# Optimization experiments

Measured on AMD Instinct MI355X. Metric: run time of the kernel, lower is better.

The kernel has to match this reference:

```python
import jax, jax.numpy as jnp
import numpy as np

N_NODES = 100000
N_EDGES = 400000
N_GRAPHS = 2048
F_IN = 78
HEADS1 = 10
OUT2 = 128


def _gat_conv(x, src, dst, W, a_src, a_dst, b, heads, out_dim):
    """PyG-style GATConv with self-loops already included in (src, dst)."""
    N = x.shape[0]
    h = (x @ W).reshape(N, heads, out_dim)                       # [N,H,D]
    alpha_src = jnp.einsum('nhd,hd->nh', h, a_src)               # [N,H]
    alpha_dst = jnp.einsum('nhd,hd->nh', h, a_dst)               # [N,H]
    e = jax.nn.leaky_relu(alpha_src[src] + alpha_dst[dst], 0.2)  # [E,H]
    # ragged softmax over incoming edges per destination node
    m = jax.ops.segment_max(e, dst, num_segments=N)
    m = jnp.where(jnp.isfinite(m), m, 0.0)
    ex = jnp.exp(e - jax.lax.stop_gradient(m)[dst])
    denom = jax.ops.segment_sum(ex, dst, num_segments=N)
    alpha = ex / (denom[dst] + 1e-16)                            # [E,H]
    msg = h[src] * alpha[:, :, None]                             # [E,H,D]
    out = jax.ops.segment_sum(msg, dst, num_segments=N)          # [N,H,D]
    return out.reshape(N, heads * out_dim) + b


def setup_inputs() -> dict:
    key = jax.random.key(0)
    ks = jax.random.split(key, 24)
    p = lambda k, shape: (jax.random.normal(k, shape, dtype=jnp.float32) * 0.05)
    x = jax.random.normal(ks[0], (N_NODES, F_IN), dtype=jnp.float32)
    edge_index = jax.random.randint(ks[1], (2, N_EDGES), 0, N_NODES, dtype=jnp.int32)
    # sorted batch assignment guaranteeing every graph is non-empty
    batch = ((jnp.arange(N_NODES, dtype=jnp.int32) * N_GRAPHS) // N_NODES).astype(jnp.int32)
    target = jax.random.normal(ks[2], (N_GRAPHS, 1280), dtype=jnp.float32)
    return {
        'x': x, 'edge_index': edge_index, 'batch': batch, 'target': target,
        'W1': p(ks[3], (F_IN, HEADS1 * F_IN)),
        'a_src1': p(ks[4], (HEADS1, F_IN)),
        'a_dst1': p(ks[5], (HEADS1, F_IN)),
        'b1': jnp.zeros((HEADS1 * F_IN,), jnp.float32),
        'W2': p(ks[6], (HEADS1 * F_IN, OUT2)),
        'a_src2': p(ks[7], (1, OUT2)),
        'a_dst2': p(ks[8], (1, OUT2)),
        'b2': jnp.zeros((OUT2,), jnp.float32),
        'w_gate': p(ks[9], (OUT2, 1)),
        'b_gate': jnp.zeros((1,), jnp.float32),
        'W_xt': p(ks[10], (1280, 256)),
        'b_xt': jnp.zeros((256,), jnp.float32),
        'W_fc1': p(ks[11], (512, 1024)),
        'b_fc1': jnp.zeros((1024,), jnp.float32),
        'W_fc2': p(ks[12], (1024, 256)),
        'b_fc2': jnp.zeros((256,), jnp.float32),
        'W_out': p(ks[13], (256, 1)),
        'b_out': jnp.zeros((1,), jnp.float32),
    }


def reference(x, edge_index, batch, target, W1, a_src1, a_dst1, b1,
              W2, a_src2, a_dst2, b2, w_gate, b_gate, W_xt, b_xt,
              W_fc1, b_fc1, W_fc2, b_fc2, W_out, b_out):
    N = x.shape[0]
    loop = jnp.arange(N, dtype=edge_index.dtype)
    src = jnp.concatenate([edge_index[0], loop])   # add self-loops (PyG default)
    dst = jnp.concatenate([edge_index[1], loop])

    h = jax.nn.elu(_gat_conv(x, src, dst, W1, a_src1, a_dst1, b1, HEADS1, F_IN))
    h = _gat_conv(h, src, dst, W2, a_src2, a_dst2, b2, 1, OUT2)
    h = jax.nn.relu(h)                              # [N,128]

    # WeightedSumAndMax readout
    w = jax.nn.sigmoid(h @ w_gate + b_gate)         # [N,1]
    h_sum = jax.ops.segment_sum(h * w, batch, num_segments=N_GRAPHS)  # [B,128]
    h_max = jax.ops.segment_max(h, batch, num_segments=N_GRAPHS)     # [B,128]
    hg = jnp.concatenate([h_sum, h_max], axis=1)    # [B,256]

    xt = target @ W_xt + b_xt                       # [B,256]
    xc = jnp.concatenate([hg, xt], axis=1)          # [B,512]
    xc = jax.nn.relu(xc @ W_fc1 + b_fc1)
    xc = jax.nn.relu(xc @ W_fc2 + b_fc2)
    return xc @ W_out + b_out                       # [B,1]
```

## Files before the change

kernel.cpp:

```cpp
#include <hip/hip_runtime.h>
#include <cstdint>
#include <cstddef>

#define N_NODESC 100000
#define N_EDGESC 400000
#define N_GRAPHSC 2048
#define F_INC 78
#define HEADS1C 10
#define D1C 78
#define F1C 780
#define OUT2C 128
#define E_TOTC (N_EDGESC + N_NODESC)

typedef unsigned short ushort_t;
typedef __attribute__((ext_vector_type(8))) short short8;
typedef __attribute__((ext_vector_type(4))) float f32x4;
typedef __attribute__((ext_vector_type(4))) unsigned int uint4v;
union U4S8 { uint4v u; short8 s; };

static __device__ __forceinline__ float lrelu(float x){ return x > 0.f ? x : 0.2f*x; }

static __device__ __forceinline__ float elu_fast(float v){
  return (v > 0.f) ? v : (__expf(v) - 1.0f);
}

static __device__ __forceinline__ unsigned short f2bf(float f){
  unsigned int u = __float_as_uint(f);
  unsigned int r = (u + 0x7fffu + ((u >> 16) & 1u)) >> 16;
  return (unsigned short)r;
}
static __device__ __forceinline__ float bf2f(unsigned short h){
  return __uint_as_float(((unsigned int)h) << 16);
}

__global__ void k_deg(const int* __restrict__ ei, int* __restrict__ deg){
  int e = blockIdx.x*256 + threadIdx.x;
  if (e >= E_TOTC) return;
  int dst = (e < N_EDGESC) ? ei[N_EDGESC + e] : (e - N_EDGESC);
  atomicAdd(&deg[dst], 1);
}

__global__ __launch_bounds__(1024) void k_scan1(const int* __restrict__ deg,
                                                int* __restrict__ rowptr,
                                                int* __restrict__ bsum){
  __shared__ int s[1024];
  int t = threadIdx.x, i = blockIdx.x*1024 + t;
  int v = (i < N_NODESC) ? deg[i] : 0;
  s[t] = v; __syncthreads();
  for (int d = 1; d < 1024; d <<= 1){
    int xv = (t >= d) ? s[t-d] : 0;
    __syncthreads();
    s[t] += xv;
    __syncthreads();
  }
  if (i < N_NODESC) rowptr[i+1] = s[t];
  if (t == 1023) bsum[blockIdx.x] = s[t];
}

__global__ void k_scan2(int* __restrict__ bsum, int* __restrict__ rowptr, int nb){
  if (threadIdx.x == 0 && blockIdx.x == 0){
    int run = 0;
    for (int b = 0; b < nb; b++){ int v = bsum[b]; bsum[b] = run; run += v; }
    rowptr[0] = 0;
  }
}

__global__ __launch_bounds__(1024) void k_scan3(int* __restrict__ rowptr,
                                                const int* __restrict__ bsum){
  int i = blockIdx.x*1024 + threadIdx.x;
  if (i < N_NODESC) rowptr[i+1] += bsum[blockIdx.x];
}

__global__ void k_scatter(const int* __restrict__ ei, const int* __restrict__ rowptr,
                          int* __restrict__ cnt, int* __restrict__ esrc){
  int e = blockIdx.x*256 + threadIdx.x;
  if (e >= E_TOTC) return;
  int src, dst;
  if (e < N_EDGESC){ src = ei[e]; dst = ei[N_EDGESC + e]; }
  else { src = dst = e - N_EDGESC; }
  int pos = rowptr[dst] + atomicAdd(&cnt[dst], 1);
  esrc[pos] = src;
}

__global__ void k_wa1(const float* __restrict__ W1, const float* __restrict__ a_src1,
                      const float* __restrict__ a_dst1, float* __restrict__ Wa1){
  int i = blockIdx.x*256 + threadIdx.x;
  if (i >= F_INC*2*HEADS1C) return;
  int d = i / (2*HEADS1C), c = i % (2*HEADS1C);
  const float* a = (c < HEADS1C) ? a_src1 : a_dst1;
  int h = (c < HEADS1C) ? c : c - HEADS1C;
  float s = 0.f;
  for (int j = 0; j < D1C; j++) s += W1[d*F1C + h*D1C + j] * a[h*D1C + j];
  Wa1[d*(2*HEADS1C) + c] = s;
}

__global__ void k_att1(const float* __restrict__ x, const float* __restrict__ Wa1,
                       float* __restrict__ att1){
  int i = blockIdx.x*256 + threadIdx.x;
  if (i >= N_NODESC*2*HEADS1C) return;
  int n = i / (2*HEADS1C), c = i % (2*HEADS1C);
  const float* xr = x + (size_t)n*F_INC;
  float s = 0.f;
  for (int d = 0; d < F_INC; d++) s += xr[d] * Wa1[d*(2*HEADS1C) + c];
  att1[i] = s;
}

__global__ void k_stats1(const float* __restrict__ att1, const int* __restrict__ rowptr,
                         const int* __restrict__ esrc, float* __restrict__ stat1){
  int i = blockIdx.x*256 + threadIdx.x;
  if (i >= N_NODESC*HEADS1C) return;
  int n = i / HEADS1C, h = i % HEADS1C;
  float ad = att1[n*20 + 10 + h];
  int b = rowptr[n], e = rowptr[n+1];
  float m = -1e30f;
  for (int p = b; p < e; p += 4){
    int c = e - p; if (c > 4) c = 4;
    float v[4];
    #pragma unroll
    for (int j = 0; j < 4; j++){ int s = esrc[p + (j < c ? j : 0)]; v[j] = att1[s*20 + h]; }
    #pragma unroll
    for (int j = 0; j < 4; j++) if (j < c) m = fmaxf(m, lrelu(v[j] + ad));
  }
  float den = 0.f;
  for (int p = b; p < e; p += 4){
    int c = e - p; if (c > 4) c = 4;
    float v[4];
    #pragma unroll
    for (int j = 0; j < 4; j++){ int s = esrc[p + (j < c ? j : 0)]; v[j] = att1[s*20 + h]; }
    #pragma unroll
    for (int j = 0; j < 4; j++) if (j < c) den += expf(lrelu(v[j] + ad) - m);
  }
  stat1[n*20 + h] = m;
  stat1[n*20 + 10 + h] = 1.f/(den + 1e-16f);
}

__global__ __launch_bounds__(64) void k_agg1(
    const float* __restrict__ x, const float* __restrict__ att1,
    const float* __restrict__ stat1, const int* __restrict__ rowptr,
    const int* __restrict__ esrc, ushort_t* __restrict__ zc, int base){
  __shared__ float xs[4][F_INC];
  __shared__ float al[4][HEADS1C];
  int n = base + blockIdx.x;
  int l = threadIdx.x;
  int b = rowptr[n], e = rowptr[n+1];
  float acc[13];
  #pragma unroll
  for (int k = 0; k < 13; k++) acc[k] = 0.f;
  int hk[13], dk[13];
  #pragma unroll
  for (int k = 0; k < 13; k++){ int f = l + 64*k; hk[k] = f/78; dk[k] = f%78; }
  float ad = 0.f, mm = 0.f, rd = 0.f;
  if (l < HEADS1C){
    ad = att1[n*20 + 10 + l];
    mm = stat1[n*20 + l];
    rd = stat1[n*20 + 10 + l];
  }
  for (int p = b; p < e; p += 4){
    int c = e - p; if (c > 4) c = 4;
    int ss[4];
    #pragma unroll
    for (int j = 0; j < 4; j++) ss[j] = esrc[p + (j < c ? j : 0)];
    if (l < 39){
      #pragma unroll
      for (int j = 0; j < 4; j++){
        float2 v = *(const float2*)(x + (size_t)ss[j]*F_INC + 2*l);
        xs[j][2*l] = v.x; xs[j][2*l+1] = v.y;
      }
    }
    if (l < HEADS1C){
      #pragma unroll
      for (int j = 0; j < 4; j++){
        float ev = lrelu(att1[ss[j]*20 + l] + ad);
        al[j][l] = (j < c) ? expf(ev - mm) * rd : 0.f;
      }
    }
    __syncthreads();
    #pragma unroll
    for (int k = 0; k < 13; k++){
      int f = l + 64*k;
      if (f < F1C){
        float s = al[0][hk[k]]*xs[0][dk[k]] + al[1][hk[k]]*xs[1][dk[k]]
                + al[2][hk[k]]*xs[2][dk[k]] + al[3][hk[k]]*xs[3][dk[k]];
        acc[k] += s;
      }
    }
    __syncthreads();
  }
  #pragma unroll
  for (int k = 0; k < 13; k++){
    int f = l + 64*k;
    if (f < F1C) zc[(size_t)blockIdx.x*F1C + f] = f2bf(acc[k]);
  }
}

__global__ void k_prepW1(const float* __restrict__ W1, ushort_t* __restrict__ W1t){
  int i = blockIdx.x*256 + threadIdx.x;
  if (i >= HEADS1C*80*96) return;
  int h = i / (80*96), rem = i % (80*96), n = rem / 96, k = rem % 96;
  float v = (n < D1C && k < F_INC) ? W1[(size_t)k*F1C + h*D1C + n] : 0.f;
  W1t[i] = f2bf(v);
}

__global__ void k_prepW2f(const float* __restrict__ W2, ushort_t* __restrict__ W2f){
  int i = blockIdx.x*256 + threadIdx.x;
  if (i >= HEADS1C*128*96) return;
  int h = i / (128*96), rem = i % (128*96), n = rem / 96, k = rem % 96;
  float v = (k < D1C) ? W2[(size_t)(h*D1C + k)*OUT2C + n] : 0.f;
  W2f[i] = f2bf(v);
}

__global__ void k_prepWt(const float* __restrict__ W, ushort_t* __restrict__ Wt,
                         int Kdim, int Ndim, int KB){
  int i = blockIdx.x*256 + threadIdx.x;
  if (i >= Ndim*KB) return;
  int n = i / KB, k = i % KB;
  float v = (k < Kdim) ? W[(size_t)k*Ndim + n] : 0.f;
  Wt[i] = f2bf(v);
}

__global__ void k_cast_bf(const float* __restrict__ in, ushort_t* __restrict__ o, int n){
  int i = blockIdx.x*256 + threadIdx.x;
  if (i < n) o[i] = f2bf(in[i]);
}

template<int BN, int NT, int KB, int KVAL, int ACT, bool HASBIAS>
__global__ __launch_bounds__(256) void mfma_gemm(
    const ushort_t* __restrict__ A, const ushort_t* __restrict__ Bt,
    const float* __restrict__ bias, ushort_t* __restrict__ C,
    int M, int N, int lda, int ldc,
    int zsA, int zsBt, int zsC, int zsBias)
{
  __shared__ unsigned int As[64][20];
  __shared__ unsigned int Bs[BN][20];
  int z = blockIdx.z;
  A += (size_t)z*zsA; Bt += (size_t)z*zsBt; C += (size_t)z*zsC;
  const float* bz = HASBIAS ? (bias + (size_t)z*zsBias) : nullptr;
  int m0 = blockIdx.x*64;
  int n0 = blockIdx.y*BN;
  int t = threadIdx.x;
  int w = t >> 6, lane = t & 63;
  int q = lane >> 4, li = lane & 15;
  f32x4 acc[NT];
  #pragma unroll
  for (int i = 0; i < NT; i++) acc[i] = (f32x4){0.f,0.f,0.f,0.f};

  int am = t >> 2;
  int ak0 = (t & 3)*8;
  int gm = m0 + am;
  bool rv = (gm < M);

  #pragma unroll
  for (int ki = 0; ki < KB/32; ki++){
    const int kt = ki*32;
    int nv;
    if (ki == KB/32 - 1){
      int d = KVAL - ak0; nv = d < 0 ? 0 : (d > 8 ? 8 : d);
    } else nv = 8;
    {
      unsigned u0=0u, u1=0u, u2=0u, u3=0u;
      if (rv && nv > 0){
        const unsigned int* ap = (const unsigned int*)(A + (size_t)gm*lda + kt + ak0);
        u0 = ap[0]; u1 = ap[1]; u2 = ap[2]; u3 = ap[3];
        int ndw = nv >> 1;
        if (ndw < 4) u3 = 0u;
        if (ndw < 3) u2 = 0u;
        if (ndw < 2) u1 = 0u;
      }
      int c0 = (t & 3)*4;
      As[am][c0] = u0; As[am][c0+1] = u1; As[am][c0+2] = u2; As[am][c0+3] = u3;
    }
    for (int g = t; g < BN*4; g += 256){
      int n = g >> 2, c0 = (g & 3)*4;
      const unsigned int* bp = (const unsigned int*)(Bt + (size_t)(n0 + n)*KB + kt + c0*2);
      Bs[n][c0] = bp[0]; Bs[n][c0+1] = bp[1]; Bs[n][c0+2] = bp[2]; Bs[n][c0+3] = bp[3];
    }
    __syncthreads();
    U4S8 a; a.u = *(const uint4v*)&As[w*16 + li][q*4];
    #pragma unroll
    for (int nt = 0; nt < NT; nt++){
      U4S8 b; b.u = *(const uint4v*)&Bs[nt*16 + li][q*4];
      acc[nt] = __builtin_amdgcn_mfma_f32_16x16x32_bf16(a.s, b.s, acc[nt], 0, 0, 0);
    }
    __syncthreads();
  }
  #pragma unroll
  for (int nt = 0; nt < NT; nt++){
    int col = n0 + nt*16 + li;
    if (col >= N) continue;
    float bv = HASBIAS ? bz[col] : 0.f;
    #pragma unroll
    for (int r = 0; r < 4; r++){
      int gmr = m0 + w*16 + q*4 + r;
      if (gmr >= M) continue;
      float v = acc[nt][r] + bv;
      if (ACT == 1) v = fmaxf(v, 0.f);
      else if (ACT == 2) v = (v > 0.f) ? v : (__expf(v) - 1.0f);
      C[(size_t)gmr*ldc + col] = f2bf(v);
    }
  }
}

__global__ __launch_bounds__(256, 4) void mfma_fused12(
    const ushort_t* __restrict__ zc, const ushort_t* __restrict__ W1t,
    const float* __restrict__ b1, const ushort_t* __restrict__ W2f,
    ushort_t* __restrict__ h2pre, float* __restrict__ att2,
    const float* __restrict__ a_src2, const float* __restrict__ a_dst2,
    int M)
{
  __shared__ unsigned int Bs[128][52];
  __shared__ unsigned int Ts[64][52];
  int m0 = blockIdx.x*64;
  int t = threadIdx.x;
  int w = t >> 6, lane = t & 63;
  int q = lane >> 4, li = lane & 15;

  f32x4 acc2[8];
  #pragma unroll
  for (int i = 0; i < 8; i++) acc2[i] = (f32x4){0.f,0.f,0.f,0.f};

  for (int i = t; i < 64*9; i += 256) Ts[i/9][39 + i%9] = 0u;

  int ar = m0 + w*16 + li;
  bool rv = (ar < M);
  const unsigned int* abase = (const unsigned int*)(zc + (size_t)ar*F1C);

  auto lda = [&](int h, uint4v* af){
    af[0] = (uint4v){0u,0u,0u,0u};
    af[1] = (uint4v){0u,0u,0u,0u};
    af[2] = (uint4v){0u,0u,0u,0u};
    if (rv){
      const unsigned int* p = abase + h*39 + q*4;
      af[0][0]=p[0];  af[0][1]=p[1];  af[0][2]=p[2];  af[0][3]=p[3];
      af[1][0]=p[16]; af[1][1]=p[17]; af[1][2]=p[18]; af[1][3]=p[19];
      if (q < 2){
        af[2][0]=p[32]; af[2][1]=p[33]; af[2][2]=p[34]; af[2][3]=p[35];
        if (q == 1) af[2][3] = 0u;
      }
    }
  };

  uint4v acur[3], anxt[3];
  lda(0, acur);

  #pragma unroll 1
  for (int h = 0; h < HEADS1C; h++){
    lda(h+1 < HEADS1C ? h+1 : 0, anxt);

    __syncthreads();
    {
      const unsigned int* bp = (const unsigned int*)(W1t + (size_t)h*80*96);
      #pragma unroll
      for (int g0 = 0; g0 < 4; g0++){
        int g = t + g0*256;
        if (g < 960){
          int n = g/12, c0 = (g%12)*4;
          const unsigned int* p = bp + g*4;
          Bs[n][c0] = p[0]; Bs[n][c0+1] = p[1]; Bs[n][c0+2] = p[2]; Bs[n][c0+3] = p[3];
        }
      }
    }
    float bv[5];
    #pragma unroll
    for (int nt = 0; nt < 5; nt++){
      int col = nt*16 + li;
      bv[nt] = (col < D1C) ? b1[h*D1C + col] : 0.f;
    }
    __syncthreads();

    f32x4 acc1[5];
    #pragma unroll
    for (int i = 0; i < 5; i++) acc1[i] = (f32x4){0.f,0.f,0.f,0.f};
    #pragma unroll
    for (int ki = 0; ki < 3; ki++){
      U4S8 a; a.u = acur[ki];
      #pragma unroll
      for (int nt = 0; nt < 5; nt++){
        U4S8 b; b.u = *(const uint4v*)&Bs[nt*16 + li][ki*16 + q*4];
        acc1[nt] = __builtin_amdgcn_mfma_f32_16x16x32_bf16(a.s, b.s, acc1[nt], 0, 0, 0);
      }
    }
    #pragma unroll
    for (int nt = 0; nt < 5; nt++){
      int col = nt*16 + li;
      #pragma unroll
      for (int r = 0; r < 4; r++){
        int row = w*16 + q*4 + r;
        float v = elu_fast(acc1[nt][r] + bv[nt]);
        ((ushort_t*)&Ts[row][0])[col] = f2bf(v);
      }
    }
    __syncthreads();

    {
      const unsigned int* bp = (const unsigned int*)(W2f + (size_t)h*128*96);
      #pragma unroll
      for (int g0 = 0; g0 < 6; g0++){
        int g = t + g0*256;
        int n = g/12, c0 = (g%12)*4;
        const unsigned int* p = bp + g*4;
        Bs[n][c0] = p[0]; Bs[n][c0+1] = p[1]; Bs[n][c0+2] = p[2]; Bs[n][c0+3] = p[3];
      }
    }
    __syncthreads();

    #pragma unroll
    for (int ki = 0; ki < 3; ki++){
      U4S8 a; a.u = *(const uint4v*)&Ts[w*16 + li][ki*16 + q*4];
      #pragma unroll
      for (int nt = 0; nt < 8; nt++){
        U4S8 b; b.u = *(const uint4v*)&Bs[nt*16 + li][ki*16 + q*4];
        acc2[nt] = __builtin_amdgcn_mfma_f32_16x16x32_bf16(a.s, b.s, acc2[nt], 0, 0, 0);
      }
    }
    acur[0] = anxt[0]; acur[1] = anxt[1]; acur[2] = anxt[2];
  }

  float as2[8], ad2[8];
  #pragma unroll
  for (int nt = 0; nt < 8; nt++){
    int col = nt*16 + li;
    as2[nt] = a_src2[col];
    ad2[nt] = a_dst2[col];
  }
  #pragma unroll
  for (int r = 0; r < 4; r++){
    int gmr = m0 + w*16 + q*4 + r;
    float p0 = 0.f, p1 = 0.f;
    ushort_t hv[8];
    #pragma unroll
    for (int nt = 0; nt < 8; nt++){
      ushort_t hb = f2bf(acc2[nt][r]);
      float vb = bf2f(hb);
      p0 += vb*as2[nt]; p1 += vb*ad2[nt];
      hv[nt] = hb;
    }
    #pragma unroll
    for (int off = 1; off < 16; off <<= 1){
      p0 += __shfl_xor(p0, off);
      p1 += __shfl_xor(p1, off);
    }
    if (gmr < M){
      #pragma unroll
      for (int nt = 0; nt < 8; nt++)
        h2pre[(size_t)gmr*OUT2C + nt*16 + li] = hv[nt];
      if (li == 0){
        att2[(size_t)gmr*2]     = p0;
        att2[(size_t)gmr*2 + 1] = p1;
      }
    }
  }
}

__global__ void k_stats2(const float* __restrict__ att2, const int* __restrict__ rowptr,
                         const int* __restrict__ esrc, float* __restrict__ stat2){
  int n = blockIdx.x*256 + threadIdx.x;
  if (n >= N_NODESC) return;
  float ad = att2[n*2+1];
  int b = rowptr[n], e = rowptr[n+1];
  float m = -1e30f;
  for (int p = b; p < e; p += 4){
    int c = e - p; if (c > 4) c = 4;
    float v[4];
    #pragma unroll
    for (int j = 0; j < 4; j++){ int s = esrc[p + (j < c ? j : 0)]; v[j] = att2[s*2]; }
    #pragma unroll
    for (int j = 0; j < 4; j++) if (j < c) m = fmaxf(m, lrelu(v[j] + ad));
  }
  float den = 0.f;
  for (int p = b; p < e; p += 4){
    int c = e - p; if (c > 4) c = 4;
    float v[4];
    #pragma unroll
    for (int j = 0; j < 4; j++){ int s = esrc[p + (j < c ? j : 0)]; v[j] = att2[s*2]; }
    #pragma unroll
    for (int j = 0; j < 4; j++) if (j < c) den += expf(lrelu(v[j] + ad) - m);
  }
  stat2[n*2] = m;
  stat2[n*2+1] = 1.f/(den + 1e-16f);
}

__global__ void k_agg2(const ushort_t* __restrict__ h2pre,
                       const float* __restrict__ att2,
                       const float* __restrict__ stat2, const int* __restrict__ rowptr,
                       const int* __restrict__ esrc, const float* __restrict__ b2,
                       const float* __restrict__ w_gate, const float* __restrict__ b_gate,
                       float* __restrict__ h2, float* __restrict__ wnode){
  int n = blockIdx.x*4 + (threadIdx.x >> 6);
  int l = threadIdx.x & 63;
  if (n >= N_NODESC) return;
  float ad = att2[n*2+1], m = stat2[n*2], rd = stat2[n*2+1];
  int b = rowptr[n], e = rowptr[n+1];
  float a0 = 0.f, a1 = 0.f;
  for (int p = b; p < e; p += 4){
    int c = e - p; if (c > 4) c = 4;
    int ss[4];
    #pragma unroll
    for (int j = 0; j < 4; j++) ss[j] = esrc[p + (j < c ? j : 0)];
    unsigned u[4]; float at[4];
    #pragma unroll
    for (int j = 0; j < 4; j++) u[j] = *(const unsigned*)(h2pre + (size_t)ss[j]*OUT2C + 2*l);
    #pragma unroll
    for (int j = 0; j < 4; j++) at[j] = att2[ss[j]*2];
    #pragma unroll
    for (int j = 0; j < 4; j++){
      if (j < c){
        float alpha = expf(lrelu(at[j] + ad) - m) * rd;
        a0 += alpha * bf2f((ushort_t)(u[j] & 0xffffu));
        a1 += alpha * bf2f((ushort_t)(u[j] >> 16));
      }
    }
  }
  float v0 = fmaxf(a0 + b2[2*l],   0.f);
  float v1 = fmaxf(a1 + b2[2*l+1], 0.f);
  float2 hv; hv.x = v0; hv.y = v1;
  *(float2*)(h2 + (size_t)n*OUT2C + 2*l) = hv;
  float pp = v0*w_gate[2*l] + v1*w_gate[2*l+1];
  #pragma unroll
  for (int off = 32; off; off >>= 1) pp += __shfl_xor(pp, off);
  if (l == 0) wnode[n] = 1.f/(1.f + expf(-(pp + b_gate[0])));
}

__global__ __launch_bounds__(128) void k_readout(const float* __restrict__ h2,
                                                 const float* __restrict__ wnode,
                                                 const int* __restrict__ batch,
                                                 ushort_t* __restrict__ xcb){
  __shared__ int lohi[2];
  int g = blockIdx.x, t = threadIdx.x;
  if (t == 0){
    int lo = 0, hi = N_NODESC;
    while (lo < hi){ int mid = (lo+hi) >> 1; if (batch[mid] < g) lo = mid+1; else hi = mid; }
    lohi[0] = lo;
    int lo2 = lo; hi = N_NODESC;
    while (lo2 < hi){ int mid = (lo2+hi) >> 1; if (batch[mid] < g+1) lo2 = mid+1; else hi = mid; }
    lohi[1] = lo2;
  }
  __syncthreads();
  int lo = lohi[0], hi = lohi[1];
  float sum = 0.f, mx = 0.f;
  for (int n = lo; n < hi; n++){
    float v = h2[(size_t)n*OUT2C + t];
    sum += v * wnode[n];
    mx = fmaxf(mx, v);
  }
  xcb[(size_t)g*512 + t] = f2bf(sum);
  xcb[(size_t)g*512 + 128 + t] = f2bf(mx);
}

__global__ void k_final(const ushort_t* __restrict__ f2b, const float* __restrict__ W_out,
                        const float* __restrict__ b_out, float* __restrict__ out){
  int g = blockIdx.x*4 + (threadIdx.x >> 6);
  int l = threadIdx.x & 63;
  if (g >= N_GRAPHSC) return;
  float s = 0.f;
  #pragma unroll
  for (int k = 0; k < 4; k++) s += bf2f(f2b[(size_t)g*256 + l + 64*k]) * W_out[l + 64*k];
  #pragma unroll
  for (int off = 32; off; off >>= 1) s += __shfl_xor(s, off);
  if (l == 0) out[g] = s + b_out[0];
}

extern "C" void kernel_launch(void* const* d_in, const int* in_sizes, int n_in,
                              void* d_out, int out_size, void* d_ws, size_t ws_size,
                              hipStream_t stream) {
  const float* x      = (const float*)d_in[0];
  const int*   ei     = (const int*)d_in[1];
  const int*   batch  = (const int*)d_in[2];
  const float* target = (const float*)d_in[3];
  const float* W1     = (const float*)d_in[4];
  const float* a_src1 = (const float*)d_in[5];
  const float* a_dst1 = (const float*)d_in[6];
  const float* b1     = (const float*)d_in[7];
  const float* W2     = (const float*)d_in[8];
  const float* a_src2 = (const float*)d_in[9];
  const float* a_dst2 = (const float*)d_in[10];
  const float* b2     = (const float*)d_in[11];
  const float* w_gate = (const float*)d_in[12];
  const float* b_gate = (const float*)d_in[13];
  const float* W_xt   = (const float*)d_in[14];
  const float* b_xt   = (const float*)d_in[15];
  const float* W_fc1  = (const float*)d_in[16];
  const float* b_fc1  = (const float*)d_in[17];
  const float* W_fc2  = (const float*)d_in[18];
  const float* b_fc2  = (const float*)d_in[19];
  const float* W_out  = (const float*)d_in[20];
  const float* b_out  = (const float*)d_in[21];
  float* out = (float*)d_out;

  const size_t MB = (size_t)1 << 20;
  int C;
  if      (ws_size >= 245*MB) C = 1;
  else if (ws_size >= 150*MB) C = 2;
  else                        C = 4;
  const int R = N_NODESC / C;

  char* p = (char*)d_ws;
  auto carve = [&](size_t bytes) -> char* {
    char* r = p; p += (bytes + 255) & ~(size_t)255; return r;
  };
  int*   deg    = (int*)  carve((size_t)N_NODESC*4);
  int*   rowptr = (int*)  carve((size_t)(N_NODESC+1)*4);
  int*   cnt    = (int*)  carve((size_t)N_NODESC*4);
  int*   esrc   = (int*)  carve((size_t)E_TOTC*4);
  int*   bsum   = (int*)  carve(128*4);
  float* Wa1    = (float*)carve((size_t)F_INC*20*4);
  float* att1   = (float*)carve((size_t)N_NODESC*20*4);
  float* stat1  = (float*)carve((size_t)N_NODESC*20*4);
  float* att2   = (float*)carve((size_t)N_NODESC*2*4);
  float* stat2  = (float*)carve((size_t)N_NODESC*2*4);
  float* wnode  = (float*)carve((size_t)N_NODESC*4);
  ushort_t* W1t   = (ushort_t*)carve((size_t)HEADS1C*80*96*2);
  ushort_t* W2f   = (ushort_t*)carve((size_t)HEADS1C*128*96*2);
  ushort_t* Wxtt  = (ushort_t*)carve((size_t)256*1280*2);
  ushort_t* Wfc1t = (ushort_t*)carve((size_t)1024*512*2);
  ushort_t* Wfc2t = (ushort_t*)carve((size_t)256*1024*2);
  ushort_t* tb    = (ushort_t*)carve((size_t)N_GRAPHSC*1280*2);
  ushort_t* h2pre = (ushort_t*)carve((size_t)N_NODESC*OUT2C*2);
  ushort_t* xcb   = (ushort_t*)carve((size_t)N_GRAPHSC*512*2);
  ushort_t* f1b   = (ushort_t*)carve((size_t)N_GRAPHSC*1024*2);
  ushort_t* f2b   = (ushort_t*)carve((size_t)N_GRAPHSC*256*2);
  size_t big_bytes = (size_t)R*F1C*2 + 4096;
  size_t h2_bytes  = (size_t)N_NODESC*OUT2C*4;
  char*  BIG = carve(big_bytes > h2_bytes ? big_bytes : h2_bytes);
  ushort_t* zc  = (ushort_t*)BIG;
  float* h2 = (float*)BIG;

  hipMemsetAsync(deg, 0, (size_t)N_NODESC*4, stream);
  hipMemsetAsync(cnt, 0, (size_t)N_NODESC*4, stream);

  k_deg<<<(E_TOTC+255)/256, 256, 0, stream>>>(ei, deg);
  int nb = (N_NODESC + 1023)/1024;
  k_scan1<<<nb, 1024, 0, stream>>>(deg, rowptr, bsum);
  k_scan2<<<1, 64, 0, stream>>>(bsum, rowptr, nb);
  k_scan3<<<nb, 1024, 0, stream>>>(rowptr, bsum);
  k_scatter<<<(E_TOTC+255)/256, 256, 0, stream>>>(ei, rowptr, cnt, esrc);

  k_prepW1<<<(HEADS1C*80*96+255)/256, 256, 0, stream>>>(W1, W1t);
  k_prepW2f<<<(HEADS1C*128*96+255)/256, 256, 0, stream>>>(W2, W2f);
  k_prepWt<<<(256*1280+255)/256, 256, 0, stream>>>(W_xt, Wxtt, 1280, 256, 1280);
  k_prepWt<<<(1024*512+255)/256, 256, 0, stream>>>(W_fc1, Wfc1t, 512, 1024, 512);
  k_prepWt<<<(256*1024+255)/256, 256, 0, stream>>>(W_fc2, Wfc2t, 1024, 256, 1024);
  k_cast_bf<<<((N_GRAPHSC*1280)+255)/256, 256, 0, stream>>>(target, tb, N_GRAPHSC*1280);

  k_wa1<<<(F_INC*20+255)/256, 256, 0, stream>>>(W1, a_src1, a_dst1, Wa1);
  k_att1<<<(N_NODESC*20+255)/256, 256, 0, stream>>>(x, Wa1, att1);
  k_stats1<<<(N_NODESC*HEADS1C+255)/256, 256, 0, stream>>>(att1, rowptr, esrc, stat1);

  for (int c = 0; c < C; c++){
    int base = c*R;
    k_agg1<<<R, 64, 0, stream>>>(x, att1, stat1, rowptr, esrc, zc, base);
    mfma_fused12<<<(R+63)/64, 256, 0, stream>>>(
        zc, W1t, b1, W2f, h2pre + (size_t)base*OUT2C, att2 + (size_t)base*2,
        a_src2, a_dst2, R);
  }

  k_stats2<<<(N_NODESC+255)/256, 256, 0, stream>>>(att2, rowptr, esrc, stat2);
  k_agg2<<<(N_NODESC+3)/4, 256, 0, stream>>>(h2pre, att2, stat2, rowptr, esrc,
                                             b2, w_gate, b_gate, h2, wnode);

  k_readout<<<N_GRAPHSC, 128, 0, stream>>>(h2, wnode, batch, xcb);
  mfma_gemm<128,8,1280,32,0,true><<<dim3(N_GRAPHSC/64, 256/128, 1), 256, 0, stream>>>(
      tb, Wxtt, b_xt, xcb + 256, N_GRAPHSC, 256, 1280, 512, 0,0,0,0);
  mfma_gemm<128,8,512,32,1,true><<<dim3(N_GRAPHSC/64, 1024/128, 1), 256, 0, stream>>>(
      xcb, Wfc1t, b_fc1, f1b, N_GRAPHSC, 1024, 512, 1024, 0,0,0,0);
  mfma_gemm<128,8,1024,32,1,true><<<dim3(N_GRAPHSC/64, 256/128, 1), 256, 0, stream>>>(
      f1b, Wfc2t, b_fc2, f2b, N_GRAPHSC, 256, 1024, 256, 0,0,0,0);
  k_final<<<(N_GRAPHSC+3)/4, 256, 0, stream>>>(f2b, W_out, b_out, out);
}
```

Measured before the change: 676.4 us.

## Prefetch per-head weight tiles into registers and use LDS-only barriers in fused GAT kernel

Weight tiles for the next stage are now loaded from global memory into registers ahead of time and written to shared memory as 128-bit vector stores after the barrier, overlapping global latency with MFMA work. Barriers are replaced with an lgkmcnt-only wait plus s_barrier, so outstanding global loads do not stall the barrier. The next-head activation prefetch is moved later in the loop. This raises register pressure under the 4-blocks-per-CU launch bound and relies on correct manual wait counts.

```diff
diff --git a/kernel.cpp b/kernel.cpp
--- a/kernel.cpp
+++ b/kernel.cpp
@@ -22,6 +22,11 @@
 
 static __device__ __forceinline__ float elu_fast(float v){
   return (v > 0.f) ? v : (__expf(v) - 1.0f);
+}
+
+static __device__ __forceinline__ void bar_lds(){
+  asm volatile("s_waitcnt lgkmcnt(0)" ::: "memory");
+  __builtin_amdgcn_s_barrier();
 }
 
 static __device__ __forceinline__ unsigned short f2bf(float f){
@@ -314,9 +319,46 @@
   int w = t >> 6, lane = t & 63;
   int q = lane >> 4, li = lane & 15;
 
+  const uint4v* w1v = (const uint4v*)W1t;
+  const uint4v* w2v = (const uint4v*)W2f;
+
+  uint4v rw1[4], rw2[6];
+  auto issueW1 = [&](int h){
+    #pragma unroll
+    for (int g0 = 0; g0 < 4; g0++){
+      int g = t + g0*256;
+      if (g < 960) rw1[g0] = w1v[(size_t)h*960 + g];
+    }
+  };
+  auto writeW1 = [&](){
+    #pragma unroll
+    for (int g0 = 0; g0 < 4; g0++){
+      int g = t + g0*256;
+      if (g < 960){
+        int n = g/12, c0 = (g%12)*4;
+        *(uint4v*)&Bs[n][c0] = rw1[g0];
+      }
+    }
+  };
+  auto issueW2 = [&](int h){
+    #pragma unroll
+    for (int g0 = 0; g0 < 6; g0++)
+      rw2[g0] = w2v[(size_t)h*1536 + t + g0*256];
+  };
+  auto writeW2 = [&](){
+    #pragma unroll
+    for (int g0 = 0; g0 < 6; g0++){
+      int g = t + g0*256;
+      int n = g/12, c0 = (g%12)*4;
+      *(uint4v*)&Bs[n][c0] = rw2[g0];
+    }
+  };
+
   f32x4 acc2[8];
   #pragma unroll
   for (int i = 0; i < 8; i++) acc2[i] = (f32x4){0.f,0.f,0.f,0.f};
+
+  issueW1(0);
 
   for (int i = t; i < 64*9; i += 256) Ts[i/9][39 + i%9] = 0u;
 
@@ -344,28 +386,16 @@
 
   #pragma unroll 1
   for (int h = 0; h < HEADS1C; h++){
-    lda(h+1 < HEADS1C ? h+1 : 0, anxt);
-
-    __syncthreads();
-    {
-      const unsigned int* bp = (const unsigned int*)(W1t + (size_t)h*80*96);
-      #pragma unroll
-      for (int g0 = 0; g0 < 4; g0++){
-        int g = t + g0*256;
-        if (g < 960){
-          int n = g/12, c0 = (g%12)*4;
-          const unsigned int* p = bp + g*4;
-          Bs[n][c0] = p[0]; Bs[n][c0+1] = p[1]; Bs[n][c0+2] = p[2]; Bs[n][c0+3] = p[3];
-        }
-      }
-    }
+    bar_lds();
+    issueW2(h);
+    writeW1();
     float bv[5];
     #pragma unroll
     for (int nt = 0; nt < 5; nt++){
       int col = nt*16 + li;
       bv[nt] = (col < D1C) ? b1[h*D1C + col] : 0.f;
     }
-    __syncthreads();
+    bar_lds();
 
     f32x4 acc1[5];
     #pragma unroll
@@ -389,19 +419,12 @@
         ((ushort_t*)&Ts[row][0])[col] = f2bf(v);
       }
     }
-    __syncthreads();
-
-    {
-      const unsigned int* bp = (const unsigned int*)(W2f + (size_t)h*128*96);
-      #pragma unroll
-      for (int g0 = 0; g0 < 6; g0++){
-        int g = t + g0*256;
-        int n = g/12, c0 = (g%12)*4;
-        const unsigned int* p = bp + g*4;
-        Bs[n][c0] = p[0]; Bs[n][c0+1] = p[1]; Bs[n][c0+2] = p[2]; Bs[n][c0+3] = p[3];
-      }
-    }
-    __syncthreads();
+    lda(h+1 < HEADS1C ? h+1 : 0, anxt);
+
+    bar_lds();
+    writeW2();
+    issueW1(h+1 < HEADS1C ? h+1 : 0);
+    bar_lds();
 
     #pragma unroll
     for (int ki = 0; ki < 3; ki++){
```

After: 663.1 us. -2.0%, faster.
